# Kernel tuning notes

Hardware: AMD Instinct MI355X
Metric: run time of the kernel (lower is better)

Reference implementation:

```python
import jax, jax.numpy as jnp
import numpy as np

N_NODES = 50000
N_EDGES = 800000
N_IN = 256
N_H = 64


def _xavier(key, fan_in, fan_out):
    limit = np.sqrt(6.0 / (fan_in + fan_out)).astype(np.float32)
    return jax.random.uniform(key, (fan_in, fan_out), jnp.float32, -limit, limit)


def setup_inputs() -> dict:
    key = jax.random.key(0)
    ks = jax.random.split(key, 12)
    inp = {
        "bf": jax.random.normal(ks[0], (1, N_NODES, N_IN), jnp.float32),
        "bl": jax.random.normal(ks[1], (1, N_NODES, N_IN), jnp.float32),
        "shuf_fts": jax.random.normal(ks[2], (1, N_NODES, N_IN), jnp.float32),
        "shuf_fls": jax.random.normal(ks[3], (1, N_NODES, N_IN), jnp.float32),
        "adj_rows": jax.random.randint(ks[4], (N_EDGES,), 0, N_NODES, jnp.int32),
        "adj_cols": jax.random.randint(ks[5], (N_EDGES,), 0, N_NODES, jnp.int32),
        "adj_w": jax.random.uniform(ks[6], (N_EDGES,), jnp.float32),
        "diff_rows": jax.random.randint(ks[7], (N_EDGES,), 0, N_NODES, jnp.int32),
        "diff_cols": jax.random.randint(ks[8], (N_EDGES,), 0, N_NODES, jnp.int32),
        "diff_w": jax.random.uniform(ks[9], (N_EDGES,), jnp.float32),
        # GCN parameters (Linear has bias=False; separate additive bias init 0; PReLU slope 0.25)
        "W1": _xavier(ks[10], N_IN, N_H),
        "b1": jnp.zeros((N_H,), jnp.float32),
        "a1": jnp.float32(0.25),
        "W2": _xavier(ks[11], N_IN, N_H),
        "b2": jnp.zeros((N_H,), jnp.float32),
        "a2": jnp.float32(0.25),
    }
    return inp


def _gcn(seq, W, b, a, rows, cols, w):
    # seq: [1, N, F_in]; sparse spmm: out[r] = sum_e 1[rows[e]==r] * w[e] * fts[cols[e]]
    fts = seq[0] @ W                                   # [N, n_h]
    msgs = w[:, None] * fts[cols]                      # [E, n_h] gather
    agg = jax.ops.segment_sum(msgs, rows, num_segments=N_NODES)  # [N, n_h] scatter-add
    out = agg[None, :, :] + b                          # bias add
    return jnp.where(out >= 0, out, a * out)           # PReLU


def reference(bf, bl, shuf_fts, shuf_fls, adj_rows, adj_cols, adj_w,
              diff_rows, diff_cols, diff_w, W1, b1, a1, W2, b2, a2):
    h_1 = _gcn(bf, W1, b1, a1, adj_rows, adj_cols, adj_w)
    h_2 = _gcn(bl, W2, b2, a2, diff_rows, diff_cols, diff_w)
    h_3 = _gcn(shuf_fts, W1, b1, a1, adj_rows, adj_cols, adj_w)
    h_4 = _gcn(shuf_fls, W2, b2, a2, diff_rows, diff_cols, diff_w)
    return jnp.stack([h_1, h_2, h_3, h_4])             # [4, 1, N, n_h]
```

## Files before the change

### kernel.cpp

```cpp
#include <hip/hip_runtime.h>
#include <hip/hip_bf16.h>

#define N_NODES 50000
#define N_EDGES 800000
#define N_IN    256
#define N_H     64
#define NB      125
#define RPB     400
#define BCAP    8192
#define EPT     8
#define BIN_BLK 2048
#define GSTRIDE 256
#define ASTRIDE 264
#define NTILES  1563
#define GEMMX   192

typedef short short8 __attribute__((ext_vector_type(8)));
typedef float f32x4  __attribute__((ext_vector_type(4)));

__device__ inline short f2bf(float f) {
    __bf16 h = (__bf16)f;
    return (short)__builtin_bit_cast(unsigned short, h);
}
__device__ inline float bflo(unsigned int q) { return __uint_as_float(q << 16); }
__device__ inline float bfhi(unsigned int q) { return __uint_as_float(q & 0xFFFF0000u); }


__global__ __launch_bounds__(256) void k_bin(
    const int* __restrict__ adj_rows, const int* __restrict__ adj_cols,
    const float* __restrict__ adj_w,
    const int* __restrict__ diff_rows, const int* __restrict__ diff_cols,
    const float* __restrict__ diff_w,
    int* __restrict__ gcnt, int2* __restrict__ bin) {

    int g = blockIdx.y;
    const int*   rows = g ? diff_rows : adj_rows;
    const int*   cols = g ? diff_cols : adj_cols;
    const float* ww   = g ? diff_w    : adj_w;
    int base_e = blockIdx.x * BIN_BLK;
    int t = threadIdx.x;

    __shared__ int lcnt[NB];
    __shared__ int lbase[NB];
    for (int i = t; i < NB; i += 256) lcnt[i] = 0;
    __syncthreads();

    int lpos[EPT];
    int bkt[EPT];
    #pragma unroll
    for (int e = 0; e < EPT; ++e) {
        int idx = base_e + e * 256 + t;
        if (idx < N_EDGES) {
            int r = rows[idx];
            int b = r / RPB;
            bkt[e] = b;
            lpos[e] = atomicAdd(&lcnt[b], 1);
        } else bkt[e] = -1;
    }
    __syncthreads();
    for (int i = t; i < NB; i += 256) lbase[i] = atomicAdd(&gcnt[g * NB + i], lcnt[i]);
    __syncthreads();

    #pragma unroll
    for (int e = 0; e < EPT; ++e) {
        int idx = base_e + e * 256 + t;
        if (idx < N_EDGES) {
            unsigned int r = (unsigned int)rows[idx];
            unsigned int c = (unsigned int)cols[idx];
            int b = bkt[e];
            int2 m;
            m.x = (int)((r << 16) | c);
            m.y = __float_as_int(ww[idx]);
            bin[((size_t)(g * NB + b)) * BCAP + lbase[b] + lpos[e]] = m;
        }
    }
}


__global__ __launch_bounds__(256) void k_build(
    const int* __restrict__ gcnt, const int2* __restrict__ bin,
    int2* __restrict__ csr, int* __restrict__ row_ptr) {

    int g = blockIdx.y, b = blockIdx.x, t = threadIdx.x;
    __shared__ int hist[512];
    __shared__ int s2[256];
    __shared__ int sbase;

    for (int i = t; i < 512; i += 256) hist[i] = 0;
    __syncthreads();

    int cnt = gcnt[g * NB + b];
    const int2* be = bin + ((size_t)(g * NB + b)) * BCAP;
    int r0 = b * RPB;

    for (int i = t; i < cnt; i += 256) {
        unsigned int rc = (unsigned int)be[i].x;
        atomicAdd(&hist[(rc >> 16) - r0], 1);
    }
    __syncthreads();

    if (t == 0) {
        int s = 0;
        for (int i = 0; i < b; ++i) s += gcnt[g * NB + i];
        sbase = s;
    }

    int v0 = hist[2 * t], v1 = hist[2 * t + 1];
    int local = v0 + v1;
    s2[t] = local;
    __syncthreads();
    for (int off = 1; off < 256; off <<= 1) {
        int v = (t >= off) ? s2[t - off] : 0;
        __syncthreads();
        s2[t] += v;
        __syncthreads();
    }
    int e0 = sbase + (s2[t] - local);
    int e1 = e0 + v0;

    int* rp = row_ptr + g * (N_NODES + 1);
    if (2 * t < RPB)     rp[r0 + 2 * t]     = e0;
    if (2 * t + 1 < RPB) rp[r0 + 2 * t + 1] = e1;
    __syncthreads();
    hist[2 * t] = e0;
    hist[2 * t + 1] = e1;
    __syncthreads();

    int2* cg = csr + (size_t)g * N_EDGES;
    for (int i = t; i < cnt; i += 256) {
        int2 m = be[i];
        unsigned int rc = (unsigned int)m.x;
        int lr = (int)(rc >> 16) - r0;
        int pos = atomicAdd(&hist[lr], 1);
        int2 o;
        o.x = (int)(rc & 0xFFFFu);
        o.y = m.y;
        cg[pos] = o;
    }
    if (b == NB - 1 && t == 0) rp[N_NODES] = N_EDGES;
}


__global__ __launch_bounds__(256) void k_wt(const float* __restrict__ W1,
                                            const float* __restrict__ W2,
                                            unsigned short* __restrict__ WTg) {
    int g = blockIdx.x;
    const float* W = g ? W2 : W1;
    unsigned short* o = WTg + (size_t)g * 64 * GSTRIDE;
    for (int i = threadIdx.x; i < N_IN * N_H; i += 256) {
        int k = i >> 6, c = i & 63;
        o[c * GSTRIDE + k] = (unsigned short)f2bf(W[i]);
    }
}


__global__ __launch_bounds__(256, 3) void k_gemm(
    const float* __restrict__ X0, const float* __restrict__ X1,
    const float* __restrict__ X2, const float* __restrict__ X3,
    const unsigned short* __restrict__ WTg,
    unsigned short* __restrict__ Tadj, unsigned short* __restrict__ Tdiff) {

    int gy = blockIdx.y;
    int g = gy >> 1, s = gy & 1;
    const float* X = g ? (s ? X3 : X1) : (s ? X2 : X0);
    unsigned short* T = g ? Tdiff : Tadj;
    const unsigned short* WB = WTg + (size_t)g * 64 * GSTRIDE;
    int coloff = s * 64;

    int t    = threadIdx.x;
    int wid  = t >> 6;
    int lane = t & 63;
    int l15  = lane & 15;
    int kg   = lane >> 4;
    int col4 = t & 63;

    __shared__ __align__(16) unsigned short A[32 * ASTRIDE];

    int ctbase = (wid >> 1) * 2;
    short8 bfr[2][8];
    #pragma unroll
    for (int c2 = 0; c2 < 2; ++c2) {
        int ct = ctbase + c2;
        #pragma unroll
        for (int kt = 0; kt < 8; ++kt) {
            bfr[c2][kt] = *reinterpret_cast<const short8*>(
                WB + ((ct * 16 + l15) * GSTRIDE + kt * 32 + kg * 8));
        }
    }

    int rt = wid & 1;
    int tile = blockIdx.x;

    float4 v[8], v2[8];
    {
        int base = tile * 32 + wid;
        #pragma unroll
        for (int j = 0; j < 8; ++j) {
            int grow = base + 4 * j; if (grow >= N_NODES) grow = N_NODES - 1;
            v[j] = ((const float4*)(X + (size_t)grow * N_IN))[col4];
        }
    }

    while (tile < NTILES) {
        int nxt = tile + GEMMX;
        if (nxt < NTILES) {
            int base = nxt * 32 + wid;
            #pragma unroll
            for (int j = 0; j < 8; ++j) {
                int grow = base + 4 * j; if (grow >= N_NODES) grow = N_NODES - 1;
                v2[j] = ((const float4*)(X + (size_t)grow * N_IN))[col4];
            }
        }
        __builtin_amdgcn_sched_barrier(0);

        #pragma unroll
        for (int j = 0; j < 8; ++j) {
            int row = wid + 4 * j;
            ushort4 c;
            c.x = (unsigned short)f2bf(v[j].x);
            c.y = (unsigned short)f2bf(v[j].y);
            c.z = (unsigned short)f2bf(v[j].z);
            c.w = (unsigned short)f2bf(v[j].w);
            *reinterpret_cast<ushort4*>(&A[row * ASTRIDE + col4 * 4]) = c;
        }
        __syncthreads();

        f32x4 acc[2];
        acc[0] = (f32x4){0.f, 0.f, 0.f, 0.f};
        acc[1] = (f32x4){0.f, 0.f, 0.f, 0.f};
        #pragma unroll
        for (int kt = 0; kt < 8; ++kt) {
            short8 af = *reinterpret_cast<const short8*>(
                &A[(rt * 16 + l15) * ASTRIDE + kt * 32 + kg * 8]);
            acc[0] = __builtin_amdgcn_mfma_f32_16x16x32_bf16(af, bfr[0][kt], acc[0], 0, 0, 0);
            acc[1] = __builtin_amdgcn_mfma_f32_16x16x32_bf16(af, bfr[1][kt], acc[1], 0, 0, 0);
        }

        int rb0 = tile * 32;
        #pragma unroll
        for (int c2 = 0; c2 < 2; ++c2) {
            int col = coloff + (ctbase + c2) * 16 + l15;
            #pragma unroll
            for (int r = 0; r < 4; ++r) {
                int row = rb0 + rt * 16 + kg * 4 + r;
                if (row < N_NODES)
                    T[(size_t)row * 128 + col] = (unsigned short)f2bf(acc[c2][r]);
            }
        }
        __syncthreads();

        tile = nxt;
        #pragma unroll
        for (int j = 0; j < 8; ++j) v[j] = v2[j];
    }
}


__global__ __launch_bounds__(256) void k_agg(
    const int* __restrict__ row_ptr, const int2* __restrict__ csr,
    const unsigned int* __restrict__ Tadj, const unsigned int* __restrict__ Tdiff,
    const float* __restrict__ b1, const float* __restrict__ a1,
    const float* __restrict__ b2, const float* __restrict__ a2,
    float* __restrict__ out) {

    int wid  = threadIdx.x >> 6;
    int lane = threadIdx.x & 63;
    int node = blockIdx.x * 4 + wid;
    int g    = blockIdx.y;

    const int* rp = row_ptr + g * (N_NODES + 1);
    const int2* el = csr + (size_t)g * N_EDGES;
    const unsigned int* Tu = g ? Tdiff : Tadj;

    int e  = rp[node];
    int e1 = rp[node + 1];
    float ax = 0.f, ay = 0.f;

    for (; e + 4 <= e1; e += 4) {
        int2 m0 = el[e + 0], m1 = el[e + 1], m2 = el[e + 2], m3 = el[e + 3];
        unsigned int q0 = Tu[(size_t)m0.x * 64 + lane];
        unsigned int q1 = Tu[(size_t)m1.x * 64 + lane];
        unsigned int q2 = Tu[(size_t)m2.x * 64 + lane];
        unsigned int q3 = Tu[(size_t)m3.x * 64 + lane];
        float w0 = __int_as_float(m0.y), w1 = __int_as_float(m1.y);
        float w2 = __int_as_float(m2.y), w3 = __int_as_float(m3.y);
        ax += w0 * bflo(q0); ay += w0 * bfhi(q0);
        ax += w1 * bflo(q1); ay += w1 * bfhi(q1);
        ax += w2 * bflo(q2); ay += w2 * bfhi(q2);
        ax += w3 * bflo(q3); ay += w3 * bfhi(q3);
    }
    for (; e < e1; ++e) {
        int2 m = el[e];
        unsigned int q = Tu[(size_t)m.x * 64 + lane];
        float w = __int_as_float(m.y);
        ax += w * bflo(q); ay += w * bfhi(q);
    }

    const float* bias = g ? b2 : b1;
    float slope = g ? a2[0] : a1[0];
    int f = 2 * lane;
    size_t base;
    int fo;
    if (lane < 32) { base = g ? (size_t)3200000 : (size_t)0;       fo = f; }
    else           { base = g ? (size_t)9600000 : (size_t)6400000; fo = f - 64; }
    float v0 = ax + bias[fo];
    float v1 = ay + bias[fo + 1];
    v0 = (v0 >= 0.f) ? v0 : slope * v0;
    v1 = (v1 >= 0.f) ? v1 : slope * v1;
    float2 res; res.x = v0; res.y = v1;
    *reinterpret_cast<float2*>(out + base + (size_t)node * 64 + fo) = res;
}


extern "C" void kernel_launch(void* const* d_in, const int* in_sizes, int n_in,
                              void* d_out, int out_size, void* d_ws, size_t ws_size,
                              hipStream_t stream) {
    const float* bf_      = (const float*)d_in[0];
    const float* bl_      = (const float*)d_in[1];
    const float* shuf_fts = (const float*)d_in[2];
    const float* shuf_fls = (const float*)d_in[3];
    const int*   adj_rows = (const int*)d_in[4];
    const int*   adj_cols = (const int*)d_in[5];
    const float* adj_w    = (const float*)d_in[6];
    const int*   diff_rows= (const int*)d_in[7];
    const int*   diff_cols= (const int*)d_in[8];
    const float* diff_w   = (const float*)d_in[9];
    const float* W1       = (const float*)d_in[10];
    const float* b1       = (const float*)d_in[11];
    const float* a1       = (const float*)d_in[12];
    const float* W2       = (const float*)d_in[13];
    const float* b2       = (const float*)d_in[14];
    const float* a2       = (const float*)d_in[15];
    float* out = (float*)d_out;

    char* ws = (char*)d_ws;
    unsigned short* Tadj  = (unsigned short*)(ws);
    unsigned short* Tdiff = (unsigned short*)(ws + 12800000);
    int2* csr             = (int2*)(ws + 25600000);
    int*  row_ptr         = (int*)(ws + 38400000);
    int*  gcnt            = (int*)(ws + 38801024);
    unsigned short* WTg   = (unsigned short*)(ws + 38803072);

    int2* bin = (int2*)d_out;

    hipMemsetAsync(gcnt, 0, 2 * NB * sizeof(int), stream);

    k_bin<<<dim3((N_EDGES + BIN_BLK - 1) / BIN_BLK, 2), dim3(256), 0, stream>>>(
        adj_rows, adj_cols, adj_w, diff_rows, diff_cols, diff_w, gcnt, bin);
    k_wt<<<dim3(2), dim3(256), 0, stream>>>(W1, W2, WTg);
    k_build<<<dim3(NB, 2), dim3(256), 0, stream>>>(gcnt, bin, csr, row_ptr);

    k_gemm<<<dim3(GEMMX, 4), dim3(256), 0, stream>>>(
        bf_, bl_, shuf_fts, shuf_fls, WTg, Tadj, Tdiff);

    k_agg<<<dim3(N_NODES / 4, 2), dim3(256), 0, stream>>>(
        row_ptr, csr, (const unsigned int*)Tadj, (const unsigned int*)Tdiff,
        b1, a1, b2, a2, out);
}
```

Before: 206.4 us.

## Fuse edge binning and feature GEMM into one launch; parallelize bucket prefix sum

Edge binning blocks and GEMM blocks now share a single kernel launch, with block index choosing the role, so the memory-bound binning runs alongside the GEMM instead of as a separate serialized launch. k_build then runs after the GEMM, since it only depends on the binning. The bucket base offset in k_build is now a parallel shared-memory tree reduction instead of a serial loop on thread 0. The fused kernel carries the GEMM's launch bounds and shared memory for every block, which may limit how many binning blocks are resident at once.

```diff
diff --git a/kernel.cpp b/kernel.cpp
--- a/kernel.cpp
+++ b/kernel.cpp
@@ -10,6 +10,7 @@
 #define BCAP    8192
 #define EPT     8
 #define BIN_BLK 2048
+#define BIN_GRID 391
 #define GSTRIDE 256
 #define ASTRIDE 264
 #define NTILES  1563
@@ -26,53 +27,170 @@
 __device__ inline float bfhi(unsigned int q) { return __uint_as_float(q & 0xFFFF0000u); }
 
 
-__global__ __launch_bounds__(256) void k_bin(
+__global__ __launch_bounds__(256) void k_wt(const float* __restrict__ W1,
+                                            const float* __restrict__ W2,
+                                            unsigned short* __restrict__ WTg) {
+    int g = blockIdx.x;
+    const float* W = g ? W2 : W1;
+    unsigned short* o = WTg + (size_t)g * 64 * GSTRIDE;
+    for (int i = threadIdx.x; i < N_IN * N_H; i += 256) {
+        int k = i >> 6, c = i & 63;
+        o[c * GSTRIDE + k] = (unsigned short)f2bf(W[i]);
+    }
+}
+
+
+__global__ __launch_bounds__(256, 3) void k_fused(
     const int* __restrict__ adj_rows, const int* __restrict__ adj_cols,
     const float* __restrict__ adj_w,
     const int* __restrict__ diff_rows, const int* __restrict__ diff_cols,
     const float* __restrict__ diff_w,
-    int* __restrict__ gcnt, int2* __restrict__ bin) {
-
-    int g = blockIdx.y;
-    const int*   rows = g ? diff_rows : adj_rows;
-    const int*   cols = g ? diff_cols : adj_cols;
-    const float* ww   = g ? diff_w    : adj_w;
-    int base_e = blockIdx.x * BIN_BLK;
+    int* __restrict__ gcnt, int2* __restrict__ bin,
+    const float* __restrict__ X0, const float* __restrict__ X1,
+    const float* __restrict__ X2, const float* __restrict__ X3,
+    const unsigned short* __restrict__ WTg,
+    unsigned short* __restrict__ Tadj, unsigned short* __restrict__ Tdiff) {
+
+    __shared__ __align__(16) unsigned short A[32 * ASTRIDE];
+
+    int fid = blockIdx.x;
     int t = threadIdx.x;
 
-    __shared__ int lcnt[NB];
-    __shared__ int lbase[NB];
-    for (int i = t; i < NB; i += 256) lcnt[i] = 0;
-    __syncthreads();
-
-    int lpos[EPT];
-    int bkt[EPT];
+    if (fid < 2 * BIN_GRID) {
+        int g = (fid >= BIN_GRID);
+        int bx = g ? (fid - BIN_GRID) : fid;
+        const int*   rows = g ? diff_rows : adj_rows;
+        const int*   cols = g ? diff_cols : adj_cols;
+        const float* ww   = g ? diff_w    : adj_w;
+        int base_e = bx * BIN_BLK;
+
+        int* lcnt  = (int*)A;
+        int* lbase = ((int*)A) + NB;
+        for (int i = t; i < NB; i += 256) lcnt[i] = 0;
+        __syncthreads();
+
+        int lpos[EPT];
+        int bkt[EPT];
+        #pragma unroll
+        for (int e = 0; e < EPT; ++e) {
+            int idx = base_e + e * 256 + t;
+            if (idx < N_EDGES) {
+                int r = rows[idx];
+                int b = r / RPB;
+                bkt[e] = b;
+                lpos[e] = atomicAdd(&lcnt[b], 1);
+            } else bkt[e] = -1;
+        }
+        __syncthreads();
+        for (int i = t; i < NB; i += 256) lbase[i] = atomicAdd(&gcnt[g * NB + i], lcnt[i]);
+        __syncthreads();
+
+        #pragma unroll
+        for (int e = 0; e < EPT; ++e) {
+            int idx = base_e + e * 256 + t;
+            if (idx < N_EDGES) {
+                unsigned int r = (unsigned int)rows[idx];
+                unsigned int c = (unsigned int)cols[idx];
+                int b = bkt[e];
+                int2 m;
+                m.x = (int)((r << 16) | c);
+                m.y = __float_as_int(ww[idx]);
+                bin[((size_t)(g * NB + b)) * BCAP + lbase[b] + lpos[e]] = m;
+            }
+        }
+        return;
+    }
+
+    int gid = fid - 2 * BIN_GRID;
+    int gy = gid & 3;
+    int g = gy >> 1, s = gy & 1;
+    const float* X = g ? (s ? X3 : X1) : (s ? X2 : X0);
+    unsigned short* T = g ? Tdiff : Tadj;
+    const unsigned short* WB = WTg + (size_t)g * 64 * GSTRIDE;
+    int coloff = s * 64;
+
+    int wid  = t >> 6;
+    int lane = t & 63;
+    int l15  = lane & 15;
+    int kg   = lane >> 4;
+    int col4 = t & 63;
+
+    int ctbase = (wid >> 1) * 2;
+    short8 bfr[2][8];
     #pragma unroll
-    for (int e = 0; e < EPT; ++e) {
-        int idx = base_e + e * 256 + t;
-        if (idx < N_EDGES) {
-            int r = rows[idx];
-            int b = r / RPB;
-            bkt[e] = b;
-            lpos[e] = atomicAdd(&lcnt[b], 1);
-        } else bkt[e] = -1;
-    }
-    __syncthreads();
-    for (int i = t; i < NB; i += 256) lbase[i] = atomicAdd(&gcnt[g * NB + i], lcnt[i]);
-    __syncthreads();
-
-    #pragma unroll
-    for (int e = 0; e < EPT; ++e) {
-        int idx = base_e + e * 256 + t;
-        if (idx < N_EDGES) {
-            unsigned int r = (unsigned int)rows[idx];
-            unsigned int c = (unsigned int)cols[idx];
-            int b = bkt[e];
-            int2 m;
-            m.x = (int)((r << 16) | c);
-            m.y = __float_as_int(ww[idx]);
-            bin[((size_t)(g * NB + b)) * BCAP + lbase[b] + lpos[e]] = m;
-        }
+    for (int c2 = 0; c2 < 2; ++c2) {
+        int ct = ctbase + c2;
+        #pragma unroll
+        for (int kt = 0; kt < 8; ++kt) {
+            bfr[c2][kt] = *reinterpret_cast<const short8*>(
+                WB + ((ct * 16 + l15) * GSTRIDE + kt * 32 + kg * 8));
+        }
+    }
+
+    int rt = wid & 1;
+    int tile = gid >> 2;
+
+    float4 v[8], v2[8];
+    {
+        int base = tile * 32 + wid;
+        #pragma unroll
+        for (int j = 0; j < 8; ++j) {
+            int grow = base + 4 * j; if (grow >= N_NODES) grow = N_NODES - 1;
+            v[j] = ((const float4*)(X + (size_t)grow * N_IN))[col4];
+        }
+    }
+
+    while (tile < NTILES) {
+        int nxt = tile + GEMMX;
+        if (nxt < NTILES) {
+            int base = nxt * 32 + wid;
+            #pragma unroll
+            for (int j = 0; j < 8; ++j) {
+                int grow = base + 4 * j; if (grow >= N_NODES) grow = N_NODES - 1;
+                v2[j] = ((const float4*)(X + (size_t)grow * N_IN))[col4];
+            }
+        }
+        __builtin_amdgcn_sched_barrier(0);
+
+        #pragma unroll
+        for (int j = 0; j < 8; ++j) {
+            int row = wid + 4 * j;
+            ushort4 c;
+            c.x = (unsigned short)f2bf(v[j].x);
+            c.y = (unsigned short)f2bf(v[j].y);
+            c.z = (unsigned short)f2bf(v[j].z);
+            c.w = (unsigned short)f2bf(v[j].w);
+            *reinterpret_cast<ushort4*>(&A[row * ASTRIDE + col4 * 4]) = c;
+        }
+        __syncthreads();
+
+        f32x4 acc[2];
+        acc[0] = (f32x4){0.f, 0.f, 0.f, 0.f};
+        acc[1] = (f32x4){0.f, 0.f, 0.f, 0.f};
+        #pragma unroll
+        for (int kt = 0; kt < 8; ++kt) {
+            short8 af = *reinterpret_cast<const short8*>(
+                &A[(rt * 16 + l15) * ASTRIDE + kt * 32 + kg * 8]);
+            acc[0] = __builtin_amdgcn_mfma_f32_16x16x32_bf16(af, bfr[0][kt], acc[0], 0, 0, 0);
+            acc[1] = __builtin_amdgcn_mfma_f32_16x16x32_bf16(af, bfr[1][kt], acc[1], 0, 0, 0);
+        }
+
+        int rb0 = tile * 32;
+        #pragma unroll
+        for (int c2 = 0; c2 < 2; ++c2) {
+            int col = coloff + (ctbase + c2) * 16 + l15;
+            #pragma unroll
+            for (int r = 0; r < 4; ++r) {
+                int row = rb0 + rt * 16 + kg * 4 + r;
+                if (row < N_NODES)
+                    T[(size_t)row * 128 + col] = (unsigned short)f2bf(acc[c2][r]);
+            }
+        }
+        __syncthreads();
+
+        tile = nxt;
+        #pragma unroll
+        for (int j = 0; j < 8; ++j) v[j] = v2[j];
     }
 }
 
@@ -97,13 +215,15 @@
         unsigned int rc = (unsigned int)be[i].x;
         atomicAdd(&hist[(rc >> 16) - r0], 1);
     }
-    __syncthreads();
-
-    if (t == 0) {
-        int s = 0;
-        for (int i = 0; i < b; ++i) s += gcnt[g * NB + i];
-        sbase = s;
-    }
+
+    s2[t] = (t < b) ? gcnt[g * NB + t] : 0;
+    __syncthreads();
+    for (int off = 128; off > 0; off >>= 1) {
+        if (t < off) s2[t] += s2[t + off];
+        __syncthreads();
+    }
+    if (t == 0) sbase = s2[0];
+    __syncthreads();
 
     int v0 = hist[2 * t], v1 = hist[2 * t + 1];
     int local = v0 + v1;
@@ -138,121 +258,6 @@
         cg[pos] = o;
     }
     if (b == NB - 1 && t == 0) rp[N_NODES] = N_EDGES;
-}
-
-
-__global__ __launch_bounds__(256) void k_wt(const float* __restrict__ W1,
-                                            const float* __restrict__ W2,
-                                            unsigned short* __restrict__ WTg) {
-    int g = blockIdx.x;
-    const float* W = g ? W2 : W1;
-    unsigned short* o = WTg + (size_t)g * 64 * GSTRIDE;
-    for (int i = threadIdx.x; i < N_IN * N_H; i += 256) {
-        int k = i >> 6, c = i & 63;
-        o[c * GSTRIDE + k] = (unsigned short)f2bf(W[i]);
-    }
-}
-
-
-__global__ __launch_bounds__(256, 3) void k_gemm(
-    const float* __restrict__ X0, const float* __restrict__ X1,
-    const float* __restrict__ X2, const float* __restrict__ X3,
-    const unsigned short* __restrict__ WTg,
-    unsigned short* __restrict__ Tadj, unsigned short* __restrict__ Tdiff) {
-
-    int gy = blockIdx.y;
-    int g = gy >> 1, s = gy & 1;
-    const float* X = g ? (s ? X3 : X1) : (s ? X2 : X0);
-    unsigned short* T = g ? Tdiff : Tadj;
-    const unsigned short* WB = WTg + (size_t)g * 64 * GSTRIDE;
-    int coloff = s * 64;
-
-    int t    = threadIdx.x;
-    int wid  = t >> 6;
-    int lane = t & 63;
-    int l15  = lane & 15;
-    int kg   = lane >> 4;
-    int col4 = t & 63;
-
-    __shared__ __align__(16) unsigned short A[32 * ASTRIDE];
-
-    int ctbase = (wid >> 1) * 2;
-    short8 bfr[2][8];
-    #pragma unroll
-    for (int c2 = 0; c2 < 2; ++c2) {
-        int ct = ctbase + c2;
-        #pragma unroll
-        for (int kt = 0; kt < 8; ++kt) {
-            bfr[c2][kt] = *reinterpret_cast<const short8*>(
-                WB + ((ct * 16 + l15) * GSTRIDE + kt * 32 + kg * 8));
-        }
-    }
-
-    int rt = wid & 1;
-    int tile = blockIdx.x;
-
-    float4 v[8], v2[8];
-    {
-        int base = tile * 32 + wid;
-        #pragma unroll
-        for (int j = 0; j < 8; ++j) {
-            int grow = base + 4 * j; if (grow >= N_NODES) grow = N_NODES - 1;
-            v[j] = ((const float4*)(X + (size_t)grow * N_IN))[col4];
-        }
-    }
-
-    while (tile < NTILES) {
-        int nxt = tile + GEMMX;
-        if (nxt < NTILES) {
-            int base = nxt * 32 + wid;
-            #pragma unroll
-            for (int j = 0; j < 8; ++j) {
-                int grow = base + 4 * j; if (grow >= N_NODES) grow = N_NODES - 1;
-                v2[j] = ((const float4*)(X + (size_t)grow * N_IN))[col4];
-            }
-        }
-        __builtin_amdgcn_sched_barrier(0);
-
-        #pragma unroll
-        for (int j = 0; j < 8; ++j) {
-            int row = wid + 4 * j;
-            ushort4 c;
-            c.x = (unsigned short)f2bf(v[j].x);
-            c.y = (unsigned short)f2bf(v[j].y);
-            c.z = (unsigned short)f2bf(v[j].z);
-            c.w = (unsigned short)f2bf(v[j].w);
-            *reinterpret_cast<ushort4*>(&A[row * ASTRIDE + col4 * 4]) = c;
-        }
-        __syncthreads();
-
-        f32x4 acc[2];
-        acc[0] = (f32x4){0.f, 0.f, 0.f, 0.f};
-        acc[1] = (f32x4){0.f, 0.f, 0.f, 0.f};
-        #pragma unroll
-        for (int kt = 0; kt < 8; ++kt) {
-            short8 af = *reinterpret_cast<const short8*>(
-                &A[(rt * 16 + l15) * ASTRIDE + kt * 32 + kg * 8]);
-            acc[0] = __builtin_amdgcn_mfma_f32_16x16x32_bf16(af, bfr[0][kt], acc[0], 0, 0, 0);
-            acc[1] = __builtin_amdgcn_mfma_f32_16x16x32_bf16(af, bfr[1][kt], acc[1], 0, 0, 0);
-        }
-
-        int rb0 = tile * 32;
-        #pragma unroll
-        for (int c2 = 0; c2 < 2; ++c2) {
-            int col = coloff + (ctbase + c2) * 16 + l15;
-            #pragma unroll
-            for (int r = 0; r < 4; ++r) {
-                int row = rb0 + rt * 16 + kg * 4 + r;
-                if (row < N_NODES)
-                    T[(size_t)row * 128 + col] = (unsigned short)f2bf(acc[c2][r]);
-            }
-        }
-        __syncthreads();
-
-        tile = nxt;
-        #pragma unroll
-        for (int j = 0; j < 8; ++j) v[j] = v2[j];
-    }
 }
 
 
@@ -345,13 +350,13 @@
 
     hipMemsetAsync(gcnt, 0, 2 * NB * sizeof(int), stream);
 
-    k_bin<<<dim3((N_EDGES + BIN_BLK - 1) / BIN_BLK, 2), dim3(256), 0, stream>>>(
-        adj_rows, adj_cols, adj_w, diff_rows, diff_cols, diff_w, gcnt, bin);
     k_wt<<<dim3(2), dim3(256), 0, stream>>>(W1, W2, WTg);
+
+    k_fused<<<dim3(2 * BIN_GRID + 4 * GEMMX), dim3(256), 0, stream>>>(
+        adj_rows, adj_cols, adj_w, diff_rows, diff_cols, diff_w, gcnt, bin,
+        bf_, bl_, shuf_fts, shuf_fls, WTg, Tadj, Tdiff);
+
     k_build<<<dim3(NB, 2), dim3(256), 0, stream>>>(gcnt, bin, csr, row_ptr);
-
-    k_gemm<<<dim3(GEMMX, 4), dim3(256), 0, stream>>>(
-        bf_, bl_, shuf_fts, shuf_fls, WTg, Tadj, Tdiff);
 
     k_agg<<<dim3(N_NODES / 4, 2), dim3(256), 0, stream>>>(
         row_ptr, csr, (const unsigned int*)Tadj, (const unsigned int*)Tdiff,
```

New measurement: 197.0 us. 1.05x faster.
